# Optimization experiments

Measured on AMD Instinct MI355X. Metric: run time of the kernel, lower is better.

Reference implementation:

```python
import jax, jax.numpy as jnp
import numpy as np

H = 500      # hidden size of RNNCell
D_IN = 512   # VGG16 feature channels
D_OUT = 100  # output vocab/logit dim
STEPS = 49   # 7x7 spatial grid consumed sequentially


def setup_inputs() -> dict:
    key = jax.random.key(0)
    ks = jax.random.split(key, 8)
    # post-VGG16 feature map for one 224x224 image: [1, 512, 7, 7]
    x = jax.random.normal(ks[0], (1, D_IN, 7, 7), dtype=jnp.float32)
    # original code uses torch.rand for the initial hidden state
    hidden0 = jax.random.uniform(ks[1], (1, H), dtype=jnp.float32)
    # nn.RNNCell(512, 500) params, PyTorch layout: W_ih [H, D_IN], W_hh [H, H]
    s_rnn = 1.0 / np.sqrt(H)
    W_ih = jax.random.uniform(ks[2], (H, D_IN), minval=-s_rnn, maxval=s_rnn, dtype=jnp.float32)
    W_hh = jax.random.uniform(ks[3], (H, H), minval=-s_rnn, maxval=s_rnn, dtype=jnp.float32)
    b_ih = jax.random.uniform(ks[4], (H,), minval=-s_rnn, maxval=s_rnn, dtype=jnp.float32)
    b_hh = jax.random.uniform(ks[5], (H,), minval=-s_rnn, maxval=s_rnn, dtype=jnp.float32)
    # nn.Linear(500, 100): W_out [D_OUT, H]
    s_out = 1.0 / np.sqrt(H)
    W_out = jax.random.uniform(ks[6], (D_OUT, H), minval=-s_out, maxval=s_out, dtype=jnp.float32)
    b_out = jax.random.uniform(ks[7], (D_OUT,), minval=-s_out, maxval=s_out, dtype=jnp.float32)
    return {"x": x, "hidden0": hidden0, "W_ih": W_ih, "W_hh": W_hh,
            "b_ih": b_ih, "b_hh": b_hh, "W_out": W_out, "b_out": b_out}


def reference(x, hidden0, W_ih, W_hh, b_ih, b_hh, W_out, b_out):
    # x: [1, 512, 7, 7] -> permute(0,2,3,1) -> [1,7,7,512] -> view(49, 1, 512)
    seq = jnp.transpose(x, (0, 2, 3, 1)).reshape(STEPS, 1, D_IN)
    # Precompute the input projection for all steps in one GEMM: [49, 1, H]
    xproj = jnp.einsum('tbd,hd->tbh', seq, W_ih) + b_ih + b_hh

    def step(h, xp):
        # h: [1, H]; RNNCell: h' = tanh(x W_ih^T + b_ih + h W_hh^T + b_hh)
        h = jnp.tanh(xp + h @ W_hh.T)
        out = jnp.tanh(h @ W_out.T + b_out)  # [1, D_OUT]
        return h, out

    _, outs = jax.lax.scan(step, hidden0, xproj)  # outs: [49, 1, 100]
    # torch.stack(op, 0).squeeze().unsqueeze(0) -> [1, 49, 100]
    return outs.squeeze(1)[None, :, :]
```

## Files before the change

kernel.cpp:

```cpp
#include <hip/hip_runtime.h>
#include <hip/hip_bf16.h>

#define H 500
#define D_IN 512
#define D_OUT 100
#define STEPS 49
#define NWG 4
#define SENT 0xFFFFFFFFu

typedef _Float16 h2_t __attribute__((ext_vector_type(2)));

#if defined(__has_builtin)
#if __has_builtin(__builtin_amdgcn_fdot2)
#define HAVE_FDOT2 1
#endif
#endif

__device__ __forceinline__ float fdot2f(h2_t a, h2_t b, float c) {
#ifdef HAVE_FDOT2
    return __builtin_amdgcn_fdot2(a, b, c, false);
#else
    return c + (float)a[0] * (float)b[0] + (float)a[1] * (float)b[1];
#endif
}
__device__ __forceinline__ h2_t bch2(unsigned u) { return __builtin_bit_cast(h2_t, u); }
__device__ __forceinline__ unsigned pk(float a, float b) {
    return __builtin_bit_cast(unsigned, h2_t{(_Float16)a, (_Float16)b});
}
__device__ __forceinline__ float tanh_fast(float x) {
    const float e = __expf(2.f * x);
    return 1.f - 2.f / (e + 1.f);
}
__device__ __forceinline__ int clen(int g) { return (g < 3) ? 128 : (H - 384); }

__global__ void k1_xproj(const float* __restrict__ x, const float* __restrict__ W_ih,
                         const float* __restrict__ b_ih, const float* __restrict__ b_hh,
                         float* __restrict__ xproj) {
    const int wv = threadIdx.x >> 6, lane = threadIdx.x & 63;
    const int r = blockIdx.x * 4 + wv;
    float wr[8];
#pragma unroll
    for (int k = 0; k < 8; k++) wr[k] = W_ih[r * D_IN + k * 64 + lane];
    float p[STEPS];
#pragma unroll
    for (int t = 0; t < STEPS; t++) p[t] = 0.f;
#pragma unroll
    for (int k = 0; k < 8; k++) {
        const float* xr = x + (size_t)(k * 64 + lane) * STEPS;
#pragma unroll
        for (int t = 0; t < STEPS; t++) p[t] = fmaf(wr[k], xr[t], p[t]);
    }
#pragma unroll
    for (int t = 0; t < STEPS; t++) {
        float v = p[t];
        v += __shfl_xor(v, 32); v += __shfl_xor(v, 16); v += __shfl_xor(v, 8);
        v += __shfl_xor(v, 4);  v += __shfl_xor(v, 2);  v += __shfl_xor(v, 1);
        p[t] = v;
    }
    if (lane == 0) {
        const float b = b_ih[r] + b_hh[r];
        for (int t = 0; t < STEPS; t++) xproj[t * 512 + r] = p[t] + b;
    }
}

__global__ void __launch_bounds__(512, 1)
k2_scan(const float* __restrict__ hidden0, const float* __restrict__ W_hh,
        const float* __restrict__ xproj, float* part, float* __restrict__ Hs) {
    __shared__ uint4 wl[16 * 512];
    __shared__ __align__(16) _Float16 hch[2][128];

    const int g = blockIdx.x, tid = threadIdx.x;
    const int rr = tid >> 2, sub = tid & 3;
    const int myLen = clen(g);

#pragma unroll
    for (int d = 0; d < 4; d++) {
        uint4 u[4] = {{0,0,0,0},{0,0,0,0},{0,0,0,0},{0,0,0,0}};
        if (rr < clen(d)) {
            const int row = 128 * d + rr;
            const float* rowp = W_hh + (size_t)row * H + 128 * g + 32 * sub;
            const int cmax = myLen - 32 * sub;
            if (cmax >= 32) {
#pragma unroll
                for (int q8 = 0; q8 < 4; q8++) {
                    const float4 f0 = *(const float4*)(rowp + 8 * q8);
                    const float4 f1 = *(const float4*)(rowp + 8 * q8 + 4);
                    u[q8].x = pk(f0.x, f0.y); u[q8].y = pk(f0.z, f0.w);
                    u[q8].z = pk(f1.x, f1.y); u[q8].w = pk(f1.z, f1.w);
                }
            } else {
                float f[32];
#pragma unroll
                for (int cc = 0; cc < 32; cc++) f[cc] = (cc < cmax) ? rowp[cc] : 0.f;
#pragma unroll
                for (int q8 = 0; q8 < 4; q8++) {
                    u[q8].x = pk(f[8*q8+0], f[8*q8+1]);
                    u[q8].y = pk(f[8*q8+2], f[8*q8+3]);
                    u[q8].z = pk(f[8*q8+4], f[8*q8+5]);
                    u[q8].w = pk(f[8*q8+6], f[8*q8+7]);
                }
            }
        }
#pragma unroll
        for (int c = 0; c < 4; c++) wl[(d * 4 + c) * 512 + tid] = u[c];
    }
    if (tid < 128) hch[0][tid] = (tid < myLen) ? (_Float16)hidden0[128 * g + tid]
                                               : (_Float16)0.f;
    else if (tid < 256) hch[1][tid - 128] = (_Float16)0.f;
    __syncthreads();

#pragma unroll 1
    for (int t = 0; t < STEPS; ++t) {
        const int cur = t & 1;
        float xp = 0.f;
        if (sub == 0 && rr < myLen) xp = xproj[t * 512 + 128 * g + rr];

        const uint4* hc = (const uint4*)&hch[cur][0];
        uint4 hv4[4];
#pragma unroll
        for (int c = 0; c < 4; c++) hv4[c] = hc[sub * 4 + c];

        float own = 0.f;
#pragma unroll
        for (int k = 0; k < 4; k++) {
            const int d = (g + 1 + k) & 3;
            float s = 0.f;
#pragma unroll
            for (int c = 0; c < 4; c++) {
                const uint4 w = wl[(d * 4 + c) * 512 + tid];
                const uint4 hb = hv4[c];
                s = fdot2f(bch2(w.x), bch2(hb.x), s);
                s = fdot2f(bch2(w.y), bch2(hb.y), s);
                s = fdot2f(bch2(w.z), bch2(hb.z), s);
                s = fdot2f(bch2(w.w), bch2(hb.w), s);
            }
            s += __shfl_xor(s, 1);
            s += __shfl_xor(s, 2);
            if (k < 3) {
                if (sub == 0)
                    __hip_atomic_store(&part[((t * 4 + d) * 4 + g) * 128 + rr], s,
                                       __ATOMIC_RELAXED, __HIP_MEMORY_SCOPE_AGENT);
            } else own = s;
        }

        if (sub == 0 && rr < myLen) {
            const int g1 = (g + 1) & 3, g2 = (g + 2) & 3, g3 = (g + 3) & 3;
            const float* pb = &part[(t * 4 + g) * 4 * 128];
            unsigned b1 = SENT, b2 = SENT, b3 = SENT;
            do {
                if (b1 == SENT) b1 = __builtin_bit_cast(unsigned,
                    __hip_atomic_load(&pb[g1 * 128 + rr], __ATOMIC_RELAXED,
                                      __HIP_MEMORY_SCOPE_AGENT));
                if (b2 == SENT) b2 = __builtin_bit_cast(unsigned,
                    __hip_atomic_load(&pb[g2 * 128 + rr], __ATOMIC_RELAXED,
                                      __HIP_MEMORY_SCOPE_AGENT));
                if (b3 == SENT) b3 = __builtin_bit_cast(unsigned,
                    __hip_atomic_load(&pb[g3 * 128 + rr], __ATOMIC_RELAXED,
                                      __HIP_MEMORY_SCOPE_AGENT));
            } while (b1 == SENT || b2 == SENT || b3 == SENT);
            const float tot = own + __builtin_bit_cast(float, b1)
                                  + __builtin_bit_cast(float, b2)
                                  + __builtin_bit_cast(float, b3) + xp;
            const float hv = tanh_fast(tot);
            Hs[t * 512 + 128 * g + rr] = hv;
            hch[cur ^ 1][rr] = (_Float16)hv;
        }
        __syncthreads();
    }
}

__global__ void k3_out(const float* __restrict__ Hs, const float* __restrict__ W_out,
                       const float* __restrict__ b_out, float* __restrict__ out) {
    const int t = blockIdx.x, o = threadIdx.x;
    if (o < D_OUT) {
        const float4* wr = (const float4*)(W_out + o * H);
        const float4* hr = (const float4*)(Hs + t * 512);
        float acc = b_out[o];
#pragma unroll 5
        for (int i = 0; i < 125; i++) {
            const float4 wv = wr[i];
            const float4 hv = hr[i];
            acc = fmaf(wv.x, hv.x, acc);
            acc = fmaf(wv.y, hv.y, acc);
            acc = fmaf(wv.z, hv.z, acc);
            acc = fmaf(wv.w, hv.w, acc);
        }
        out[t * D_OUT + o] = tanh_fast(acc);
    }
}

extern "C" void kernel_launch(void* const* d_in, const int* in_sizes, int n_in,
                              void* d_out, int out_size, void* d_ws, size_t ws_size,
                              hipStream_t stream) {
    const float* x       = (const float*)d_in[0];
    const float* hidden0 = (const float*)d_in[1];
    const float* W_ih    = (const float*)d_in[2];
    const float* W_hh    = (const float*)d_in[3];
    const float* b_ih    = (const float*)d_in[4];
    const float* b_hh    = (const float*)d_in[5];
    const float* W_out   = (const float*)d_in[6];
    const float* b_out   = (const float*)d_in[7];
    float* out = (float*)d_out;

    char* ws = (char*)d_ws;
    float* part  = (float*)ws;
    float* xproj = (float*)(ws + 401408);
    float* Hs    = (float*)(ws + 501760);

    hipMemsetAsync(part, 0xFF, 401408, stream);
    k1_xproj<<<125, 256, 0, stream>>>(x, W_ih, b_ih, b_hh, xproj);
    k2_scan<<<NWG, 512, 0, stream>>>(hidden0, W_hh, xproj, part, Hs);
    k3_out<<<STEPS, 128, 0, stream>>>(Hs, W_out, b_out, out);
}
```

Measured before the change: 103.6 us.

## Fuse xproj, scan and output kernels into one launch with flag-based dataflow

```diff
diff --git a/kernel.cpp b/kernel.cpp
--- a/kernel.cpp
+++ b/kernel.cpp
@@ -6,6 +6,8 @@
 #define D_OUT 100
 #define STEPS 49
 #define NWG 4
+#define NPROD 63
+#define NBLK (NWG + NPROD + STEPS)
 #define SENT 0xFFFFFFFFu
 
 typedef _Float16 h2_t __attribute__((ext_vector_type(2)));
@@ -32,44 +34,85 @@
     return 1.f - 2.f / (e + 1.f);
 }
 __device__ __forceinline__ int clen(int g) { return (g < 3) ? 128 : (H - 384); }
-
-__global__ void k1_xproj(const float* __restrict__ x, const float* __restrict__ W_ih,
-                         const float* __restrict__ b_ih, const float* __restrict__ b_hh,
-                         float* __restrict__ xproj) {
-    const int wv = threadIdx.x >> 6, lane = threadIdx.x & 63;
-    const int r = blockIdx.x * 4 + wv;
-    float wr[8];
-#pragma unroll
-    for (int k = 0; k < 8; k++) wr[k] = W_ih[r * D_IN + k * 64 + lane];
-    float p[STEPS];
-#pragma unroll
-    for (int t = 0; t < STEPS; t++) p[t] = 0.f;
-#pragma unroll
-    for (int k = 0; k < 8; k++) {
-        const float* xr = x + (size_t)(k * 64 + lane) * STEPS;
-#pragma unroll
-        for (int t = 0; t < STEPS; t++) p[t] = fmaf(wr[k], xr[t], p[t]);
-    }
-#pragma unroll
-    for (int t = 0; t < STEPS; t++) {
-        float v = p[t];
-        v += __shfl_xor(v, 32); v += __shfl_xor(v, 16); v += __shfl_xor(v, 8);
-        v += __shfl_xor(v, 4);  v += __shfl_xor(v, 2);  v += __shfl_xor(v, 1);
-        p[t] = v;
-    }
-    if (lane == 0) {
-        const float b = b_ih[r] + b_hh[r];
-        for (int t = 0; t < STEPS; t++) xproj[t * 512 + r] = p[t] + b;
-    }
+__device__ __forceinline__ unsigned aload(const float* p) {
+    return __builtin_bit_cast(unsigned,
+        __hip_atomic_load(p, __ATOMIC_RELAXED, __HIP_MEMORY_SCOPE_AGENT));
+}
+__device__ __forceinline__ void astore(float* p, float v) {
+    __hip_atomic_store(p, v, __ATOMIC_RELAXED, __HIP_MEMORY_SCOPE_AGENT);
 }
 
 __global__ void __launch_bounds__(512, 1)
-k2_scan(const float* __restrict__ hidden0, const float* __restrict__ W_hh,
-        const float* __restrict__ xproj, float* part, float* __restrict__ Hs) {
+k_fused(const float* __restrict__ hidden0, const float* __restrict__ W_hh,
+        const float* __restrict__ x, const float* __restrict__ W_ih,
+        const float* __restrict__ b_ih, const float* __restrict__ b_hh,
+        const float* __restrict__ W_out, const float* __restrict__ b_out,
+        float* part, float* xproj, float* Hs, float* __restrict__ out) {
     __shared__ uint4 wl[16 * 512];
     __shared__ __align__(16) _Float16 hch[2][128];
 
-    const int g = blockIdx.x, tid = threadIdx.x;
+    const int tid = threadIdx.x;
+    const int bid = blockIdx.x;
+
+    if (bid >= NWG && bid < NWG + NPROD) {
+        const int p = bid - NWG;
+        const int wv = tid >> 6, lane = tid & 63;
+        const int r = p * 8 + wv;
+        if (r >= H) return;
+        float wr8[8];
+#pragma unroll
+        for (int k = 0; k < 8; k++) wr8[k] = W_ih[r * D_IN + k * 64 + lane];
+        float pv[STEPS];
+#pragma unroll
+        for (int t = 0; t < STEPS; t++) pv[t] = 0.f;
+#pragma unroll
+        for (int k = 0; k < 8; k++) {
+            const float* xr = x + (size_t)(k * 64 + lane) * STEPS;
+#pragma unroll
+            for (int t = 0; t < STEPS; t++) pv[t] = fmaf(wr8[k], xr[t], pv[t]);
+        }
+#pragma unroll
+        for (int t = 0; t < STEPS; t++) {
+            float v = pv[t];
+            v += __shfl_xor(v, 32); v += __shfl_xor(v, 16); v += __shfl_xor(v, 8);
+            v += __shfl_xor(v, 4);  v += __shfl_xor(v, 2);  v += __shfl_xor(v, 1);
+            pv[t] = v;
+        }
+        if (lane == 0) {
+            const float b = b_ih[r] + b_hh[r];
+            for (int t = 0; t < STEPS; t++) astore(&xproj[t * 512 + r], pv[t] + b);
+        }
+        return;
+    }
+
+    if (bid >= NWG) {
+        const int t = bid - NWG - NPROD;
+        float* hsm = (float*)wl;
+        if (tid < H) {
+            unsigned hb;
+            do { hb = aload(&Hs[t * 512 + tid]); } while (hb == SENT);
+            hsm[tid] = __builtin_bit_cast(float, hb);
+        }
+        __syncthreads();
+        if (tid < D_OUT) {
+            const float4* wr = (const float4*)(W_out + tid * H);
+            const float4* hr = (const float4*)hsm;
+            float acc = b_out[tid];
+#pragma unroll 5
+            for (int i = 0; i < 125; i++) {
+                const float4 wv = wr[i];
+                const float4 hv = hr[i];
+                acc = fmaf(wv.x, hv.x, acc);
+                acc = fmaf(wv.y, hv.y, acc);
+                acc = fmaf(wv.z, hv.z, acc);
+                acc = fmaf(wv.w, hv.w, acc);
+            }
+            out[t * D_OUT + tid] = tanh_fast(acc);
+        }
+        return;
+    }
+
+    const int g = bid;
     const int rr = tid >> 2, sub = tid & 3;
     const int myLen = clen(g);
 
@@ -112,8 +155,9 @@
 #pragma unroll 1
     for (int t = 0; t < STEPS; ++t) {
         const int cur = t & 1;
-        float xp = 0.f;
-        if (sub == 0 && rr < myLen) xp = xproj[t * 512 + 128 * g + rr];
+        unsigned xb = SENT;
+        const float* xpp = &xproj[t * 512 + 128 * g + rr];
+        if (sub == 0 && rr < myLen) xb = aload(xpp);
 
         const uint4* hc = (const uint4*)&hch[cur][0];
         uint4 hv4[4];
@@ -138,8 +182,7 @@
             s += __shfl_xor(s, 2);
             if (k < 3) {
                 if (sub == 0)
-                    __hip_atomic_store(&part[((t * 4 + d) * 4 + g) * 128 + rr], s,
-                                       __ATOMIC_RELAXED, __HIP_MEMORY_SCOPE_AGENT);
+                    astore(&part[((t * 4 + d) * 4 + g) * 128 + rr], s);
             } else own = s;
         }
 
@@ -148,44 +191,20 @@
             const float* pb = &part[(t * 4 + g) * 4 * 128];
             unsigned b1 = SENT, b2 = SENT, b3 = SENT;
             do {
-                if (b1 == SENT) b1 = __builtin_bit_cast(unsigned,
-                    __hip_atomic_load(&pb[g1 * 128 + rr], __ATOMIC_RELAXED,
-                                      __HIP_MEMORY_SCOPE_AGENT));
-                if (b2 == SENT) b2 = __builtin_bit_cast(unsigned,
-                    __hip_atomic_load(&pb[g2 * 128 + rr], __ATOMIC_RELAXED,
-                                      __HIP_MEMORY_SCOPE_AGENT));
-                if (b3 == SENT) b3 = __builtin_bit_cast(unsigned,
-                    __hip_atomic_load(&pb[g3 * 128 + rr], __ATOMIC_RELAXED,
-                                      __HIP_MEMORY_SCOPE_AGENT));
+                if (b1 == SENT) b1 = aload(&pb[g1 * 128 + rr]);
+                if (b2 == SENT) b2 = aload(&pb[g2 * 128 + rr]);
+                if (b3 == SENT) b3 = aload(&pb[g3 * 128 + rr]);
             } while (b1 == SENT || b2 == SENT || b3 == SENT);
+            while (xb == SENT) xb = aload(xpp);
             const float tot = own + __builtin_bit_cast(float, b1)
                                   + __builtin_bit_cast(float, b2)
-                                  + __builtin_bit_cast(float, b3) + xp;
+                                  + __builtin_bit_cast(float, b3)
+                                  + __builtin_bit_cast(float, xb);
             const float hv = tanh_fast(tot);
-            Hs[t * 512 + 128 * g + rr] = hv;
+            astore(&Hs[t * 512 + 128 * g + rr], hv);
             hch[cur ^ 1][rr] = (_Float16)hv;
         }
         __syncthreads();
-    }
-}
-
-__global__ void k3_out(const float* __restrict__ Hs, const float* __restrict__ W_out,
-                       const float* __restrict__ b_out, float* __restrict__ out) {
-    const int t = blockIdx.x, o = threadIdx.x;
-    if (o < D_OUT) {
-        const float4* wr = (const float4*)(W_out + o * H);
-        const float4* hr = (const float4*)(Hs + t * 512);
-        float acc = b_out[o];
-#pragma unroll 5
-        for (int i = 0; i < 125; i++) {
-            const float4 wv = wr[i];
-            const float4 hv = hr[i];
-            acc = fmaf(wv.x, hv.x, acc);
-            acc = fmaf(wv.y, hv.y, acc);
-            acc = fmaf(wv.z, hv.z, acc);
-            acc = fmaf(wv.w, hv.w, acc);
-        }
-        out[t * D_OUT + o] = tanh_fast(acc);
     }
 }
 
@@ -207,8 +226,7 @@
     float* xproj = (float*)(ws + 401408);
     float* Hs    = (float*)(ws + 501760);
 
-    hipMemsetAsync(part, 0xFF, 401408, stream);
-    k1_xproj<<<125, 256, 0, stream>>>(x, W_ih, b_ih, b_hh, xproj);
-    k2_scan<<<NWG, 512, 0, stream>>>(hidden0, W_hh, xproj, part, Hs);
-    k3_out<<<STEPS, 128, 0, stream>>>(Hs, W_out, b_out, out);
-}
+    hipMemsetAsync(ws, 0xFF, 602112, stream);
+    k_fused<<<NBLK, 512, 0, stream>>>(hidden0, W_hh, x, W_ih, b_ih, b_hh,
+                                      W_out, b_out, part, xproj, Hs, out);
+}
```

Measured after the change: 107.3 us. 3.5% more time.
